# Kernel optimization log

Measured on AMD Instinct MI355X. Metric: run time of the kernel, lower is better.

Reference implementation:

```python
import jax, jax.numpy as jnp
import numpy as np

N_NODES = 50000
N_EDGES = 800000
IN_CH = 1024
OUT_CH = 256


def setup_inputs() -> dict:
    key = jax.random.key(0)
    ks = jax.random.split(key, 7)
    x = jax.random.normal(ks[0], (N_NODES, IN_CH), dtype=jnp.float32)
    src_index = jax.random.randint(ks[1], (N_EDGES,), 0, N_NODES, dtype=jnp.int32)
    tar_index = jax.random.randint(ks[2], (N_EDGES,), 0, N_NODES, dtype=jnp.int32)
    edge_weight = jax.random.uniform(ks[3], (N_EDGES,), dtype=jnp.float32)
    self_edge_weight = jax.random.uniform(ks[4], (N_NODES,), dtype=jnp.float32)
    # Linear layer params (torch.nn.Linear: y = x @ W.T + b)
    bound = 1.0 / np.sqrt(IN_CH)
    W = jax.random.uniform(ks[5], (OUT_CH, IN_CH), dtype=jnp.float32, minval=-bound, maxval=bound)
    b = jax.random.uniform(ks[6], (OUT_CH,), dtype=jnp.float32, minval=-bound, maxval=bound)
    return {"x": x, "W": W, "b": b, "src_index": src_index, "tar_index": tar_index,
            "edge_weight": edge_weight, "self_edge_weight": self_edge_weight}


def reference(x, W, b, src_index, tar_index, edge_weight, self_edge_weight):
    # dense linear projection: [N, in] -> [N, out]
    h = jnp.einsum('ni,oi->no', x, W) + b
    # edge aggregation: out[t] += w_e * h[src_e]  (SpMM-like gather/scatter)
    msgs = h[src_index] * edge_weight[:, None]          # [E, out]
    agg = jax.ops.segment_sum(msgs, tar_index, num_segments=h.shape[0])
    # self-loop term
    return agg + self_edge_weight[:, None] * h
```

## Files before the change

kernel.cpp:

```cpp
#include <hip/hip_runtime.h>
#include <hip/hip_bf16.h>

#define N_NODES 50000
#define N_EDGES 800000
#define IN_CH 1024
#define OUT_CH 256
#define NBLK 196

typedef __attribute__((ext_vector_type(8))) short bf16x8;
typedef __attribute__((ext_vector_type(4))) float f32x4;

__device__ inline unsigned short f2bf(float f) {
  union { float f; unsigned int u; } v; v.f = f;
  unsigned int r = v.u + 0x7fffu + ((v.u >> 16) & 1u);
  return (unsigned short)(r >> 16);
}
__device__ inline float bf2f(unsigned short u) {
  union { unsigned int u; float f; } v; v.u = ((unsigned int)u) << 16;
  return v.f;
}

__global__ __launch_bounds__(256) void prep(const float* __restrict__ W,
                                            unsigned short* __restrict__ Wb,
                                            int* __restrict__ counts) {
  const int b = blockIdx.x, t = threadIdx.x;
  if (b < 256) {
    const int i4 = (b * 256 + t) * 4;
    float4 f = *(const float4*)(W + i4);
    *(ushort4*)(Wb + i4) = make_ushort4(f2bf(f.x), f2bf(f.y), f2bf(f.z), f2bf(f.w));
  } else {
    const int i = (b - 256) * 256 + t;
    if (i < N_NODES) counts[i] = 0;
  }
}

__global__ __launch_bounds__(256) void gemm_proj(
    const float* __restrict__ X, const unsigned short* __restrict__ Wb,
    const float* __restrict__ bias, unsigned short* __restrict__ Hb)
{
  __shared__ unsigned short lds_a[2][128][32];
  __shared__ unsigned short lds_b[2][128][32];

  const int tid  = threadIdx.x;
  const int lane = tid & 63;
  const int w    = tid >> 6;
  const int wr   = w >> 1, wc = w & 1;
  const int gm0  = blockIdx.x * 128;
  const int gn0  = blockIdx.y * 128;

  const int arow0 = tid >> 3;
  const int acol  = (tid & 7) * 4;
  const int brow0 = tid >> 2;
  const int bq8   = (tid & 3) * 8;

  f32x4 acc[4][4];
  #pragma unroll
  for (int i = 0; i < 4; i++)
    #pragma unroll
    for (int j = 0; j < 4; j++) acc[i][j] = (f32x4)0.0f;

  float4 av[4];
  bf16x8 bv[2];

#define LOAD_STEP(K0)                                                          \
  {                                                                            \
    _Pragma("unroll")                                                          \
    for (int r = 0; r < 4; r++) {                                              \
      const int grow = gm0 + arow0 + r * 32;                                   \
      av[r] = (grow < N_NODES)                                                 \
                  ? *(const float4*)(X + (size_t)grow * IN_CH + (K0) + acol)   \
                  : make_float4(0.f, 0.f, 0.f, 0.f);                           \
    }                                                                          \
    _Pragma("unroll")                                                          \
    for (int r = 0; r < 2; r++) {                                              \
      const int wrow = gn0 + brow0 + r * 64;                                   \
      bv[r] = *(const bf16x8*)(Wb + (size_t)wrow * IN_CH + (K0) + bq8);        \
    }                                                                          \
  }

#define WRITE_STEP(BUF)                                                        \
  {                                                                            \
    _Pragma("unroll")                                                          \
    for (int r = 0; r < 4; r++)                                                \
      *(ushort4*)&lds_a[BUF][arow0 + r * 32][acol] =                           \
          make_ushort4(f2bf(av[r].x), f2bf(av[r].y), f2bf(av[r].z),            \
                       f2bf(av[r].w));                                         \
    _Pragma("unroll")                                                          \
    for (int r = 0; r < 2; r++)                                                \
      *(bf16x8*)&lds_b[BUF][brow0 + r * 64][bq8] = bv[r];                      \
  }

  LOAD_STEP(0);
  WRITE_STEP(0);
  __syncthreads();

  int buf = 0;
  for (int ks = 0; ks < IN_CH / 32; ks++) {
    if (ks + 1 < IN_CH / 32) LOAD_STEP((ks + 1) * 32);

    bf16x8 af[4], bfr[4];
    const int kq8 = (lane >> 4) * 8;
    #pragma unroll
    for (int i = 0; i < 4; i++)
      af[i] = *(const bf16x8*)&lds_a[buf][wr * 64 + i * 16 + (lane & 15)][kq8];
    #pragma unroll
    for (int j = 0; j < 4; j++)
      bfr[j] = *(const bf16x8*)&lds_b[buf][wc * 64 + j * 16 + (lane & 15)][kq8];

    #pragma unroll
    for (int i = 0; i < 4; i++)
      #pragma unroll
      for (int j = 0; j < 4; j++)
        acc[i][j] = __builtin_amdgcn_mfma_f32_16x16x32_bf16(af[i], bfr[j], acc[i][j], 0, 0, 0);

    if (ks + 1 < IN_CH / 32) WRITE_STEP(buf ^ 1);
    __syncthreads();
    buf ^= 1;
  }
#undef LOAD_STEP
#undef WRITE_STEP

  #pragma unroll
  for (int i = 0; i < 4; i++) {
    const int grow_base = gm0 + wr * 64 + i * 16 + ((lane >> 4) << 2);
    #pragma unroll
    for (int r = 0; r < 4; r++) {
      const int grow = grow_base + r;
      if (grow < N_NODES) {
        #pragma unroll
        for (int j = 0; j < 4; j++) {
          const int gcol = gn0 + wc * 64 + j * 16 + (lane & 15);
          Hb[(size_t)grow * OUT_CH + gcol] = f2bf(acc[i][j][r] + bias[gcol]);
        }
      }
    }
  }
}

__global__ __launch_bounds__(256) void hist_kernel(const int* __restrict__ tar,
                                                   int* __restrict__ counts) {
  int e = blockIdx.x * blockDim.x + threadIdx.x;
  if (e < N_EDGES) atomicAdd(&counts[tar[e]], 1);
}

__global__ __launch_bounds__(256) void scan_block(const int* __restrict__ counts,
                                                  int* __restrict__ offsets,
                                                  int* __restrict__ blocksum) {
  __shared__ int wsum[4];
  const int tid = threadIdx.x, lane = tid & 63, wv = tid >> 6;
  const int i = blockIdx.x * 256 + tid;
  const int v = (i < N_NODES) ? counts[i] : 0;
  int s = v;
  #pragma unroll
  for (int off = 1; off < 64; off <<= 1) {
    int t = __shfl_up(s, off, 64);
    if (lane >= off) s += t;
  }
  if (lane == 63) wsum[wv] = s;
  __syncthreads();
  if (tid == 0) {
    int c = 0;
    #pragma unroll
    for (int k = 0; k < 4; k++) { int t = wsum[k]; wsum[k] = c; c += t; }
  }
  __syncthreads();
  const int excl = wsum[wv] + s - v;
  if (i < N_NODES) offsets[i] = excl;
  if (tid == 255) blocksum[blockIdx.x] = excl + v;
}

__global__ __launch_bounds__(256) void scan_sums(int* __restrict__ blocksum,
                                                 int* __restrict__ offsets) {
  __shared__ int wsum[4];
  const int tid = threadIdx.x, lane = tid & 63, wv = tid >> 6;
  const int v = (tid < NBLK) ? blocksum[tid] : 0;
  int s = v;
  #pragma unroll
  for (int off = 1; off < 64; off <<= 1) {
    int t = __shfl_up(s, off, 64);
    if (lane >= off) s += t;
  }
  if (lane == 63) wsum[wv] = s;
  __syncthreads();
  if (tid == 0) {
    int c = 0;
    #pragma unroll
    for (int k = 0; k < 4; k++) { int t = wsum[k]; wsum[k] = c; c += t; }
  }
  __syncthreads();
  const int excl = wsum[wv] + s - v;
  if (tid < NBLK) blocksum[tid] = excl;
  if (tid == 255) offsets[N_NODES] = excl;
}

__global__ __launch_bounds__(256) void finalize_offsets(int* __restrict__ offsets,
                                                        const int* __restrict__ blocksum,
                                                        int* __restrict__ cursor) {
  const int i = blockIdx.x * 256 + threadIdx.x;
  if (i < N_NODES) {
    const int off = offsets[i] + blocksum[i >> 8];
    offsets[i] = off;
    cursor[i] = off;
  }
}

__global__ __launch_bounds__(256) void fill_csr(const int* __restrict__ src,
                                                const int* __restrict__ tar,
                                                const float* __restrict__ ew,
                                                int* __restrict__ cursor,
                                                int2* __restrict__ edata) {
  int e = blockIdx.x * blockDim.x + threadIdx.x;
  if (e >= N_EDGES) return;
  const int t = tar[e];
  const int p = atomicAdd(&cursor[t], 1);
  edata[p] = make_int2(src[e], __float_as_int(ew[e]));
}

__global__ __launch_bounds__(256) void node_agg(
    const unsigned short* __restrict__ Hb, const int* __restrict__ offsets,
    const int2* __restrict__ edata, const float* __restrict__ sw,
    float* __restrict__ OUT)
{
  const int wid = (blockIdx.x * blockDim.x + threadIdx.x) >> 6;
  if (wid >= N_NODES) return;
  const int lane = threadIdx.x & 63;
  const int e0 = offsets[wid];
  const int e1 = offsets[wid + 1];

  float a0 = 0.f, a1 = 0.f, a2 = 0.f, a3 = 0.f;

  for (int base = e0; base < e1; base += 64) {
    const int avail = e1 - base;
    int2 d = make_int2(0, 0);
    if (lane < avail) d = edata[base + lane];
    const int n = (avail < 64) ? avail : 64;
    int j = 0;
    for (; j + 4 <= n; j += 4) {
      const int   s0 = __shfl(d.x, j, 64),     s1 = __shfl(d.x, j + 1, 64);
      const int   s2 = __shfl(d.x, j + 2, 64), s3 = __shfl(d.x, j + 3, 64);
      const float w0 = __int_as_float(__shfl(d.y, j, 64));
      const float w1 = __int_as_float(__shfl(d.y, j + 1, 64));
      const float w2 = __int_as_float(__shfl(d.y, j + 2, 64));
      const float w3 = __int_as_float(__shfl(d.y, j + 3, 64));
      const ushort4 h0 = *(const ushort4*)(Hb + (size_t)s0 * OUT_CH + lane * 4);
      const ushort4 h1 = *(const ushort4*)(Hb + (size_t)s1 * OUT_CH + lane * 4);
      const ushort4 h2 = *(const ushort4*)(Hb + (size_t)s2 * OUT_CH + lane * 4);
      const ushort4 h3 = *(const ushort4*)(Hb + (size_t)s3 * OUT_CH + lane * 4);
      a0 += w0 * bf2f(h0.x) + w1 * bf2f(h1.x) + w2 * bf2f(h2.x) + w3 * bf2f(h3.x);
      a1 += w0 * bf2f(h0.y) + w1 * bf2f(h1.y) + w2 * bf2f(h2.y) + w3 * bf2f(h3.y);
      a2 += w0 * bf2f(h0.z) + w1 * bf2f(h1.z) + w2 * bf2f(h2.z) + w3 * bf2f(h3.z);
      a3 += w0 * bf2f(h0.w) + w1 * bf2f(h1.w) + w2 * bf2f(h2.w) + w3 * bf2f(h3.w);
    }
    for (; j < n; j++) {
      const int   s = __shfl(d.x, j, 64);
      const float wgt = __int_as_float(__shfl(d.y, j, 64));
      const ushort4 h = *(const ushort4*)(Hb + (size_t)s * OUT_CH + lane * 4);
      a0 += wgt * bf2f(h.x); a1 += wgt * bf2f(h.y);
      a2 += wgt * bf2f(h.z); a3 += wgt * bf2f(h.w);
    }
  }

  const float swv = sw[wid];
  const ushort4 hs = *(const ushort4*)(Hb + (size_t)wid * OUT_CH + lane * 4);
  float4 o;
  o.x = a0 + swv * bf2f(hs.x);
  o.y = a1 + swv * bf2f(hs.y);
  o.z = a2 + swv * bf2f(hs.z);
  o.w = a3 + swv * bf2f(hs.w);
  *(float4*)(OUT + (size_t)wid * OUT_CH + lane * 4) = o;
}

extern "C" void kernel_launch(void* const* d_in, const int* in_sizes, int n_in,
                              void* d_out, int out_size, void* d_ws, size_t ws_size,
                              hipStream_t stream) {
  const float* x   = (const float*)d_in[0];
  const float* W   = (const float*)d_in[1];
  const float* b   = (const float*)d_in[2];
  const int*   src = (const int*)d_in[3];
  const int*   tar = (const int*)d_in[4];
  const float* ew  = (const float*)d_in[5];
  const float* sw  = (const float*)d_in[6];
  float* out = (float*)d_out;

  char* ws = (char*)d_ws;
  size_t o = 0;
  unsigned short* Wb = (unsigned short*)(ws + o);
  o += (size_t)OUT_CH * IN_CH * 2;          o = (o + 255) & ~(size_t)255;
  unsigned short* Hb = (unsigned short*)(ws + o);
  o += (size_t)N_NODES * OUT_CH * 2;        o = (o + 255) & ~(size_t)255;
  int* counts   = (int*)(ws + o); o += (size_t)N_NODES * 4;       o = (o + 255) & ~(size_t)255;
  int* offsets  = (int*)(ws + o); o += (size_t)(N_NODES + 1) * 4; o = (o + 255) & ~(size_t)255;
  int* cursor   = (int*)(ws + o); o += (size_t)N_NODES * 4;       o = (o + 255) & ~(size_t)255;
  int* blocksum = (int*)(ws + o); o += (size_t)NBLK * 4;          o = (o + 255) & ~(size_t)255;
  int2* edata   = (int2*)(ws + o);

  prep<<<256 + NBLK, 256, 0, stream>>>(W, Wb, counts);

  dim3 g1((N_NODES + 127) / 128, OUT_CH / 128);
  gemm_proj<<<g1, 256, 0, stream>>>(x, Wb, b, Hb);

  hist_kernel<<<(N_EDGES + 255) / 256, 256, 0, stream>>>(tar, counts);
  scan_block<<<NBLK, 256, 0, stream>>>(counts, offsets, blocksum);
  scan_sums<<<1, 256, 0, stream>>>(blocksum, offsets);
  finalize_offsets<<<NBLK, 256, 0, stream>>>(offsets, blocksum, cursor);
  fill_csr<<<(N_EDGES + 255) / 256, 256, 0, stream>>>(src, tar, ew, cursor, edata);

  const long long nthreads = (long long)N_NODES * 64;
  node_agg<<<(int)((nthreads + 255) / 256), 256, 0, stream>>>(Hb, offsets, edata, sw, out);
}
```

Before: 245.3 us.

## Shrink GEMM tile to 64 rows, fuse histogram into prep, reorder launches

The projection GEMM now uses a 64x128 block tile with 2x4 MFMA tiles per wave, launch bounds allowing 4 blocks per CU, precomputed row pointers, a 2-stage unrolled register/LDS double buffer, and bias hoisted into registers. This gives more blocks (about 1564 vs 782) to fill the CUs, at the cost of less reuse of W per X load. The edge histogram is folded into the weight conversion kernel, with counts cleared by a memset, which removes one launch. The CSR build now runs before the GEMM.

```diff
diff --git a/kernel.cpp b/kernel.cpp
--- a/kernel.cpp
+++ b/kernel.cpp
@@ -20,109 +20,122 @@
   return v.f;
 }
 
-__global__ __launch_bounds__(256) void prep(const float* __restrict__ W,
-                                            unsigned short* __restrict__ Wb,
-                                            int* __restrict__ counts) {
+__global__ __launch_bounds__(256) void prep_hist(const float* __restrict__ W,
+                                                 unsigned short* __restrict__ Wb,
+                                                 const int* __restrict__ tar,
+                                                 int* __restrict__ counts) {
   const int b = blockIdx.x, t = threadIdx.x;
   if (b < 256) {
     const int i4 = (b * 256 + t) * 4;
     float4 f = *(const float4*)(W + i4);
     *(ushort4*)(Wb + i4) = make_ushort4(f2bf(f.x), f2bf(f.y), f2bf(f.z), f2bf(f.w));
   } else {
-    const int i = (b - 256) * 256 + t;
-    if (i < N_NODES) counts[i] = 0;
-  }
-}
-
-__global__ __launch_bounds__(256) void gemm_proj(
+    const int e = (b - 256) * 256 + t;
+    if (e < N_EDGES) atomicAdd(&counts[tar[e]], 1);
+  }
+}
+
+__global__ __launch_bounds__(256, 4) void gemm_proj(
     const float* __restrict__ X, const unsigned short* __restrict__ Wb,
     const float* __restrict__ bias, unsigned short* __restrict__ Hb)
 {
-  __shared__ unsigned short lds_a[2][128][32];
+  __shared__ unsigned short lds_a[2][64][32];
   __shared__ unsigned short lds_b[2][128][32];
 
   const int tid  = threadIdx.x;
   const int lane = tid & 63;
   const int w    = tid >> 6;
   const int wr   = w >> 1, wc = w & 1;
-  const int gm0  = blockIdx.x * 128;
+  const int gm0  = blockIdx.x * 64;
   const int gn0  = blockIdx.y * 128;
 
-  const int arow0 = tid >> 3;
-  const int acol  = (tid & 7) * 4;
-  const int brow0 = tid >> 2;
-  const int bq8   = (tid & 3) * 8;
-
-  f32x4 acc[4][4];
-  #pragma unroll
-  for (int i = 0; i < 4; i++)
+  const int ar = tid >> 3;
+  const int ac = (tid & 7) * 4;
+  const int br = tid >> 2;
+  const int bc = (tid & 3) * 8;
+
+  const int arow0 = gm0 + ar, arow1 = gm0 + ar + 32;
+  const bool aok0 = arow0 < N_NODES, aok1 = arow1 < N_NODES;
+  const float* xp0 = X + (size_t)arow0 * IN_CH + ac;
+  const float* xp1 = X + (size_t)arow1 * IN_CH + ac;
+  const unsigned short* wp0 = Wb + (size_t)(gn0 + br) * IN_CH + bc;
+  const unsigned short* wp1 = Wb + (size_t)(gn0 + br + 64) * IN_CH + bc;
+
+  f32x4 acc[2][4];
+  #pragma unroll
+  for (int i = 0; i < 2; i++)
     #pragma unroll
     for (int j = 0; j < 4; j++) acc[i][j] = (f32x4)0.0f;
 
-  float4 av[4];
-  bf16x8 bv[2];
-
-#define LOAD_STEP(K0)                                                          \
+  float4 avA0, avA1, avB0, avB1;
+  bf16x8 bvA0, bvA1, bvB0, bvB1;
+
+#define LOADR(KS, AV0, AV1, BV0, BV1)                                          \
   {                                                                            \
-    _Pragma("unroll")                                                          \
-    for (int r = 0; r < 4; r++) {                                              \
-      const int grow = gm0 + arow0 + r * 32;                                   \
-      av[r] = (grow < N_NODES)                                                 \
-                  ? *(const float4*)(X + (size_t)grow * IN_CH + (K0) + acol)   \
-                  : make_float4(0.f, 0.f, 0.f, 0.f);                           \
-    }                                                                          \
-    _Pragma("unroll")                                                          \
-    for (int r = 0; r < 2; r++) {                                              \
-      const int wrow = gn0 + brow0 + r * 64;                                   \
-      bv[r] = *(const bf16x8*)(Wb + (size_t)wrow * IN_CH + (K0) + bq8);        \
-    }                                                                          \
-  }
-
-#define WRITE_STEP(BUF)                                                        \
+    const int k0_ = (KS) * 32;                                                 \
+    AV0 = aok0 ? *(const float4*)(xp0 + k0_) : make_float4(0.f, 0.f, 0.f, 0.f);\
+    AV1 = aok1 ? *(const float4*)(xp1 + k0_) : make_float4(0.f, 0.f, 0.f, 0.f);\
+    BV0 = *(const bf16x8*)(wp0 + k0_);                                         \
+    BV1 = *(const bf16x8*)(wp1 + k0_);                                         \
+  }
+
+#define WRITER(BUF, AV0, AV1, BV0, BV1)                                        \
   {                                                                            \
-    _Pragma("unroll")                                                          \
-    for (int r = 0; r < 4; r++)                                                \
-      *(ushort4*)&lds_a[BUF][arow0 + r * 32][acol] =                           \
-          make_ushort4(f2bf(av[r].x), f2bf(av[r].y), f2bf(av[r].z),            \
-                       f2bf(av[r].w));                                         \
-    _Pragma("unroll")                                                          \
-    for (int r = 0; r < 2; r++)                                                \
-      *(bf16x8*)&lds_b[BUF][brow0 + r * 64][bq8] = bv[r];                      \
-  }
-
-  LOAD_STEP(0);
-  WRITE_STEP(0);
-  __syncthreads();
-
-  int buf = 0;
-  for (int ks = 0; ks < IN_CH / 32; ks++) {
-    if (ks + 1 < IN_CH / 32) LOAD_STEP((ks + 1) * 32);
-
-    bf16x8 af[4], bfr[4];
-    const int kq8 = (lane >> 4) * 8;
-    #pragma unroll
-    for (int i = 0; i < 4; i++)
-      af[i] = *(const bf16x8*)&lds_a[buf][wr * 64 + i * 16 + (lane & 15)][kq8];
-    #pragma unroll
-    for (int j = 0; j < 4; j++)
-      bfr[j] = *(const bf16x8*)&lds_b[buf][wc * 64 + j * 16 + (lane & 15)][kq8];
-
-    #pragma unroll
-    for (int i = 0; i < 4; i++)
-      #pragma unroll
-      for (int j = 0; j < 4; j++)
-        acc[i][j] = __builtin_amdgcn_mfma_f32_16x16x32_bf16(af[i], bfr[j], acc[i][j], 0, 0, 0);
-
-    if (ks + 1 < IN_CH / 32) WRITE_STEP(buf ^ 1);
+    *(ushort4*)&lds_a[BUF][ar][ac] =                                           \
+        make_ushort4(f2bf(AV0.x), f2bf(AV0.y), f2bf(AV0.z), f2bf(AV0.w));      \
+    *(ushort4*)&lds_a[BUF][ar + 32][ac] =                                      \
+        make_ushort4(f2bf(AV1.x), f2bf(AV1.y), f2bf(AV1.z), f2bf(AV1.w));      \
+    *(bf16x8*)&lds_b[BUF][br][bc]      = BV0;                                  \
+    *(bf16x8*)&lds_b[BUF][br + 64][bc] = BV1;                                  \
+  }
+
+#define COMPUTE(BUF)                                                           \
+  {                                                                            \
+    const int l15_ = lane & 15;                                                \
+    const int kb_  = (lane >> 4) * 8;                                          \
+    bf16x8 a0 = *(const bf16x8*)&lds_a[BUF][wr * 32 + l15_][kb_];              \
+    bf16x8 a1 = *(const bf16x8*)&lds_a[BUF][wr * 32 + 16 + l15_][kb_];         \
+    bf16x8 b0 = *(const bf16x8*)&lds_b[BUF][wc * 64 + l15_][kb_];              \
+    bf16x8 b1 = *(const bf16x8*)&lds_b[BUF][wc * 64 + 16 + l15_][kb_];         \
+    bf16x8 b2 = *(const bf16x8*)&lds_b[BUF][wc * 64 + 32 + l15_][kb_];         \
+    bf16x8 b3 = *(const bf16x8*)&lds_b[BUF][wc * 64 + 48 + l15_][kb_];         \
+    acc[0][0] = __builtin_amdgcn_mfma_f32_16x16x32_bf16(a0, b0, acc[0][0], 0, 0, 0); \
+    acc[0][1] = __builtin_amdgcn_mfma_f32_16x16x32_bf16(a0, b1, acc[0][1], 0, 0, 0); \
+    acc[0][2] = __builtin_amdgcn_mfma_f32_16x16x32_bf16(a0, b2, acc[0][2], 0, 0, 0); \
+    acc[0][3] = __builtin_amdgcn_mfma_f32_16x16x32_bf16(a0, b3, acc[0][3], 0, 0, 0); \
+    acc[1][0] = __builtin_amdgcn_mfma_f32_16x16x32_bf16(a1, b0, acc[1][0], 0, 0, 0); \
+    acc[1][1] = __builtin_amdgcn_mfma_f32_16x16x32_bf16(a1, b1, acc[1][1], 0, 0, 0); \
+    acc[1][2] = __builtin_amdgcn_mfma_f32_16x16x32_bf16(a1, b2, acc[1][2], 0, 0, 0); \
+    acc[1][3] = __builtin_amdgcn_mfma_f32_16x16x32_bf16(a1, b3, acc[1][3], 0, 0, 0); \
+  }
+
+  LOADR(0, avA0, avA1, bvA0, bvA1);
+  WRITER(0, avA0, avA1, bvA0, bvA1);
+  LOADR(1, avB0, avB1, bvB0, bvB1);
+  __syncthreads();
+
+  for (int ks = 0; ks < 32; ks += 2) {
+    if (ks + 2 < 32) LOADR(ks + 2, avA0, avA1, bvA0, bvA1);
+    COMPUTE(0);
+    WRITER(1, avB0, avB1, bvB0, bvB1);
     __syncthreads();
-    buf ^= 1;
-  }
-#undef LOAD_STEP
-#undef WRITE_STEP
-
-  #pragma unroll
-  for (int i = 0; i < 4; i++) {
-    const int grow_base = gm0 + wr * 64 + i * 16 + ((lane >> 4) << 2);
+    if (ks + 3 < 32) LOADR(ks + 3, avB0, avB1, bvB0, bvB1);
+    COMPUTE(1);
+    if (ks + 2 < 32) WRITER(0, avA0, avA1, bvA0, bvA1);
+    __syncthreads();
+  }
+#undef LOADR
+#undef WRITER
+#undef COMPUTE
+
+  float bj[4];
+  #pragma unroll
+  for (int j = 0; j < 4; j++)
+    bj[j] = bias[gn0 + wc * 64 + j * 16 + (lane & 15)];
+
+  #pragma unroll
+  for (int i = 0; i < 2; i++) {
+    const int grow_base = gm0 + wr * 32 + i * 16 + ((lane >> 4) << 2);
     #pragma unroll
     for (int r = 0; r < 4; r++) {
       const int grow = grow_base + r;
@@ -130,17 +143,11 @@
         #pragma unroll
         for (int j = 0; j < 4; j++) {
           const int gcol = gn0 + wc * 64 + j * 16 + (lane & 15);
-          Hb[(size_t)grow * OUT_CH + gcol] = f2bf(acc[i][j][r] + bias[gcol]);
+          Hb[(size_t)grow * OUT_CH + gcol] = f2bf(acc[i][j][r] + bj[j]);
         }
       }
     }
   }
-}
-
-__global__ __launch_bounds__(256) void hist_kernel(const int* __restrict__ tar,
-                                                   int* __restrict__ counts) {
-  int e = blockIdx.x * blockDim.x + threadIdx.x;
-  if (e < N_EDGES) atomicAdd(&counts[tar[e]], 1);
 }
 
 __global__ __launch_bounds__(256) void scan_block(const int* __restrict__ counts,
@@ -294,17 +301,16 @@
   int* blocksum = (int*)(ws + o); o += (size_t)NBLK * 4;          o = (o + 255) & ~(size_t)255;
   int2* edata   = (int2*)(ws + o);
 
-  prep<<<256 + NBLK, 256, 0, stream>>>(W, Wb, counts);
-
-  dim3 g1((N_NODES + 127) / 128, OUT_CH / 128);
-  gemm_proj<<<g1, 256, 0, stream>>>(x, Wb, b, Hb);
-
-  hist_kernel<<<(N_EDGES + 255) / 256, 256, 0, stream>>>(tar, counts);
+  hipMemsetAsync(counts, 0, (size_t)N_NODES * 4, stream);
+  prep_hist<<<256 + (N_EDGES + 255) / 256, 256, 0, stream>>>(W, Wb, tar, counts);
   scan_block<<<NBLK, 256, 0, stream>>>(counts, offsets, blocksum);
   scan_sums<<<1, 256, 0, stream>>>(blocksum, offsets);
   finalize_offsets<<<NBLK, 256, 0, stream>>>(offsets, blocksum, cursor);
   fill_csr<<<(N_EDGES + 255) / 256, 256, 0, stream>>>(src, tar, ew, cursor, edata);
 
+  dim3 g1((N_NODES + 63) / 64, OUT_CH / 128);
+  gemm_proj<<<g1, 256, 0, stream>>>(x, Wb, b, Hb);
+
   const long long nthreads = (long long)N_NODES * 64;
   node_agg<<<(int)((nthreads + 255) / 256), 256, 0, stream>>>(Hb, offsets, edata, sw, out);
 }
```

New measurement: 244.0 us. No clear change (-0.5%).
